# Kernel optimization log

Hardware: AMD Instinct MI355X
Metric: run time of the kernel (lower is better)

Reference implementation:

```python
import jax, jax.numpy as jnp
import numpy as np

CHAN = 24
INNER = 64
GROUPS = 8
M = 5
LAM = 1e-4
MAX_ITER = 25
BETA = 1.0
EPS = 1e-5
B, HH, WW = 128, 32, 32


def conv2d(x, w, b=None):
    # NCHW, OIHW, 3x3 SAME conv (padding = kernel//2)
    y = jax.lax.conv_general_dilated(x, w, (1, 1), 'SAME',
                                     dimension_numbers=('NCHW', 'OIHW', 'NCHW'))
    if b is not None:
        y = y + b[None, :, None, None]
    return y


def group_norm(x, g, b):
    bsz, c, h, w = x.shape
    xg = x.reshape(bsz, GROUPS, c // GROUPS, h, w)
    mu = xg.mean(axis=(2, 3, 4), keepdims=True)
    var = xg.var(axis=(2, 3, 4), keepdims=True)
    xn = ((xg - mu) / jnp.sqrt(var + EPS)).reshape(bsz, c, h, w)
    return xn * g[None, :, None, None] + b[None, :, None, None]


def batch_norm(x, g, b):
    # training-mode batch statistics over (N, H, W)
    mu = x.mean(axis=(0, 2, 3), keepdims=True)
    var = x.var(axis=(0, 2, 3), keepdims=True)
    return (x - mu) / jnp.sqrt(var + EPS) * g[None, :, None, None] + b[None, :, None, None]


def resnet_f(p, z, x):
    c1w, g1g, g1b, c2w, g2g, g2b, g3g, g3b = p
    y = group_norm(jax.nn.relu(conv2d(z, c1w)), g1g, g1b)
    return group_norm(jax.nn.relu(z + group_norm(x + conv2d(y, c2w), g2g, g2b)), g3g, g3b)


def anderson(f, x0):
    # Anderson acceleration, fixed MAX_ITER iterations (no host-sync tol break).
    bsz = x0.shape[0]
    d = x0.size // bsz
    X = jnp.zeros((bsz, M, d), x0.dtype)
    Fm = jnp.zeros((bsz, M, d), x0.dtype)
    f0 = f(x0).reshape(bsz, -1)
    X = X.at[:, 0].set(x0.reshape(bsz, -1))
    Fm = Fm.at[:, 0].set(f0)
    X = X.at[:, 1].set(f0)
    Fm = Fm.at[:, 1].set(f(f0.reshape(x0.shape)).reshape(bsz, -1))
    for k in range(2, MAX_ITER):
        n = min(k, M)
        G = Fm[:, :n] - X[:, :n]                       # [b, n, d]
        Hm = jnp.zeros((bsz, n + 1, n + 1), x0.dtype)
        Hm = Hm.at[:, 0, 1:].set(1.0).at[:, 1:, 0].set(1.0)
        Hm = Hm.at[:, 1:, 1:].set(jnp.einsum('bnd,bmd->bnm', G, G)
                                  + LAM * jnp.eye(n, dtype=x0.dtype)[None])
        yv = jnp.zeros((bsz, n + 1, 1), x0.dtype).at[:, 0, 0].set(1.0)
        alpha = jnp.linalg.solve(Hm, yv)[:, 1:, 0]     # [b, n]
        xnew = (BETA * jnp.einsum('bn,bnd->bd', alpha, Fm[:, :n])
                + (1.0 - BETA) * jnp.einsum('bn,bnd->bd', alpha, X[:, :n]))
        X = X.at[:, k % M].set(xnew)
        Fm = Fm.at[:, k % M].set(f(xnew.reshape(x0.shape)).reshape(bsz, -1))
    return X[:, (MAX_ITER - 1) % M].reshape(x0.shape)


def setup_inputs() -> dict:
    key = jax.random.key(0)
    ks = jax.random.split(key, 8)
    inp = {
        'x': jax.random.normal(ks[0], (B, 3, HH, WW), jnp.float32),
        'pre_conv_w': jax.random.normal(ks[1], (CHAN, 3, 3, 3), jnp.float32) * 0.1,
        'pre_conv_b': jnp.zeros((CHAN,), jnp.float32),
        'pre_bn_g': jnp.ones((CHAN,), jnp.float32),
        'pre_bn_b': jnp.zeros((CHAN,), jnp.float32),
        'f_conv1_w': jax.random.normal(ks[2], (INNER, CHAN, 3, 3), jnp.float32) * 0.01,
        'gn1_g': jnp.ones((INNER,), jnp.float32),
        'gn1_b': jnp.zeros((INNER,), jnp.float32),
        'f_conv2_w': jax.random.normal(ks[3], (CHAN, INNER, 3, 3), jnp.float32) * 0.01,
        'gn2_g': jnp.ones((CHAN,), jnp.float32),
        'gn2_b': jnp.zeros((CHAN,), jnp.float32),
        'gn3_g': jnp.ones((CHAN,), jnp.float32),
        'gn3_b': jnp.zeros((CHAN,), jnp.float32),
        'post_bn_g': jnp.ones((CHAN,), jnp.float32),
        'post_bn_b': jnp.zeros((CHAN,), jnp.float32),
        'fc_w': jax.random.normal(ks[4], (10, CHAN * 4 * 4), jnp.float32) * 0.05,
        'fc_b': jnp.zeros((10,), jnp.float32),
    }
    return inp


def reference(x, pre_conv_w, pre_conv_b, pre_bn_g, pre_bn_b,
              f_conv1_w, gn1_g, gn1_b, f_conv2_w, gn2_g, gn2_b, gn3_g, gn3_b,
              post_bn_g, post_bn_b, fc_w, fc_b):
    # pre: conv + BatchNorm
    xp = batch_norm(conv2d(x, pre_conv_w, pre_conv_b), pre_bn_g, pre_bn_b)
    p = (f_conv1_w, gn1_g, gn1_b, f_conv2_w, gn2_g, gn2_b, gn3_g, gn3_b)
    # DEQ fixed-point solve (eval path: train=False returns the fixed point)
    z_star = anderson(lambda z: resnet_f(p, z, xp), jnp.zeros_like(xp))
    z = resnet_f(p, z_star, xp)
    # post: relu -> BN -> avgpool(8,8) -> flatten -> linear
    h = batch_norm(jax.nn.relu(z), post_bn_g, post_bn_b)
    bsz, c, hh, ww = h.shape
    pooled = h.reshape(bsz, c, hh // 8, 8, ww // 8, 8).mean(axis=(3, 5))  # [B,C,4,4]
    return pooled.reshape(bsz, -1) @ fc_w.T + fc_b
```

## Files before the change

### kernel.cpp

```cpp
#include <hip/hip_runtime.h>
#include <hip/hip_bf16.h>

typedef __hip_bfloat16 bf16;
typedef unsigned short ushortT;
typedef __attribute__((ext_vector_type(8))) short short8;
typedef __attribute__((ext_vector_type(4))) float f32x4;

#define BB 128
#define CHAN 24
#define INNER 64
#define HW 1024
#define DD (CHAN*HW)

constexpr size_t cBD = (size_t)BB*DD;
constexpr size_t cYB = (size_t)BB*INNER*HW;

__device__ __attribute__((aligned(16))) ushortT g_xp[cBD];
__device__ __attribute__((aligned(16))) ushortT g_X[5*cBD];
__device__ __attribute__((aligned(16))) ushortT g_F[5*cBD];
__device__ __attribute__((aligned(16))) ushortT g_G[5*cBD];
__device__ __attribute__((aligned(16))) ushortT g_yb[cYB];
__device__ __attribute__((aligned(16))) ushortT g_tb[cBD];
__device__ __attribute__((aligned(16))) ushortT g_w1m[9*64*32];
__device__ __attribute__((aligned(16))) ushortT g_w2m[9*24*64];
__device__ __attribute__((aligned(16))) float g_stats2a[48];
__device__ __attribute__((aligned(16))) float g_stats2b[48];
__device__ __attribute__((aligned(16))) float g_gn1sum[BB*8*2];
__device__ __attribute__((aligned(16))) float g_gram[BB*25];
__device__ __attribute__((aligned(16))) float g_params[5120];
__device__ unsigned g_isbf16;

#define P_PCW 0
#define P_PCB 648
#define P_PBG 672
#define P_PBB 696
#define P_G1G 720
#define P_G1B 784
#define P_G2G 848
#define P_G2B 872
#define P_G3G 896
#define P_G3B 920
#define P_POG 944
#define P_POB 968
#define P_FCW 992
#define P_FCB 4832

__device__ __forceinline__ size_t aidx(int b, int icv, int pix){
  return (((size_t)b*3 + icv)*1024 + (size_t)pix)*8;
}
__device__ __forceinline__ float rdin(const void* p, int i){
  if (g_isbf16) return __bfloat162float(((const bf16*)p)[i]);
  return ((const float*)p)[i];
}
__device__ __forceinline__ float b2f(ushortT u){
  unsigned v = ((unsigned)u) << 16;
  return __builtin_bit_cast(float, v);
}
__device__ __forceinline__ ushortT f2b(float f){
  unsigned u = __builtin_bit_cast(unsigned, f);
  u += 0x7FFFu + ((u >> 16) & 1u);
  return (ushortT)(u >> 16);
}
__device__ __forceinline__ void ld24c(const ushortT* base, int b, int pix, float* o){
  #pragma unroll
  for (int icv=0;icv<3;icv++){
    short8 v = *(const short8*)&base[aidx(b,icv,pix)];
    #pragma unroll
    for (int j=0;j<8;j++) o[icv*8+j] = b2f((ushortT)v[j]);
  }
}
__device__ __forceinline__ void st24c(ushortT* base, int b, int pix, const float* i){
  #pragma unroll
  for (int icv=0;icv<3;icv++){
    short8 v;
    #pragma unroll
    for (int j=0;j<8;j++) v[j] = (short)f2b(i[icv*8+j]);
    *(short8*)&base[aidx(b,icv,pix)] = v;
  }
}

__global__ void detect_k(const void* g1g){
  if (threadIdx.x==0 && blockIdx.x==0){
    unsigned u = *(const unsigned*)g1g;
    g_isbf16 = (u == 0x3F803F80u) ? 1u : 0u;
  }
}

__global__ void cvt_params_k(const void* pcw, const void* pcb, const void* pbg, const void* pbb,
                             const void* g1g, const void* g1b, const void* g2g, const void* g2b,
                             const void* g3g, const void* g3b, const void* pog, const void* pob,
                             const void* fcw, const void* fcb){
  int t = threadIdx.x;
  for (int i=t;i<648;i+=256)  g_params[P_PCW+i]=rdin(pcw,i);
  for (int i=t;i<24;i+=256) { g_params[P_PCB+i]=rdin(pcb,i);
                              g_params[P_PBG+i]=rdin(pbg,i);
                              g_params[P_PBB+i]=rdin(pbb,i);
                              g_params[P_G2G+i]=rdin(g2g,i);
                              g_params[P_G2B+i]=rdin(g2b,i);
                              g_params[P_G3G+i]=rdin(g3g,i);
                              g_params[P_G3B+i]=rdin(g3b,i);
                              g_params[P_POG+i]=rdin(pog,i);
                              g_params[P_POB+i]=rdin(pob,i); }
  for (int i=t;i<64;i+=256) { g_params[P_G1G+i]=rdin(g1g,i);
                              g_params[P_G1B+i]=rdin(g1b,i); }
  for (int i=t;i<3840;i+=256) g_params[P_FCW+i]=rdin(fcw,i);
  for (int i=t;i<10;i+=256)   g_params[P_FCB+i]=rdin(fcb,i);
  for (int i=t;i<48;i+=256) { g_stats2a[i]=0.f; g_stats2b[i]=0.f; }
}

__global__ void wtm_k(const void* w1, const void* w2){
  int t = blockIdx.x*256 + threadIdx.x;
  if (t < 9*64*32){
    int ic = t & 31, oc = (t>>5)&63, s9 = t>>11;
    float v = (ic<24) ? rdin(w1, (oc*24+ic)*9 + s9) : 0.f;
    g_w1m[t] = f2b(v);
  }
  int u = t - 9*64*32;
  if (u >= 0 && u < 9*24*64){
    int ic = u & 63; int rest = u >> 6; int oc = rest % 24; int s9 = rest / 24;
    g_w2m[u] = f2b(rdin(w2, (oc*64+ic)*9 + s9));
  }
}

__global__ void zero0_k(){
  size_t base = ((size_t)blockIdx.x*256 + threadIdx.x)*8;
  short8 z = {0,0,0,0,0,0,0,0};
  *(short8*)&g_yb[base] = z;
  if (blockIdx.x < 1536) *(short8*)&g_X[base] = z;
  int t = blockIdx.x*256 + threadIdx.x;
  if (blockIdx.x < 8)  g_gn1sum[t] = 0.f;
}

__global__ void preconv_k(const void* __restrict__ x){
  __shared__ float sR2d[4*48];
  int id = blockIdx.x*256 + threadIdx.x;
  int b = id >> 10, pix = id & 1023;
  int yy = pix >> 5, xx = pix & 31;
  float acc[24];
  #pragma unroll
  for (int oc=0;oc<24;oc++) acc[oc] = g_params[P_PCB+oc];
  for (int ic=0; ic<3; ic++)
    for (int ky=0; ky<3; ky++){
      int gy = yy+ky-1; if (gy<0||gy>=32) continue;
      for (int kx=0;kx<3;kx++){
        int gx = xx+kx-1; if (gx<0||gx>=32) continue;
        float v = rdin(x, ((b*3+ic)*32+gy)*32+gx);
        #pragma unroll
        for (int oc=0;oc<24;oc++)
          acc[oc] += v * g_params[P_PCW+(oc*3+ic)*9+ky*3+kx];
      }
    }
  st24c(g_tb, b, pix, acc);
  int lane = threadIdx.x & 63, wv = threadIdx.x >> 6;
  #pragma unroll
  for (int c=0;c<24;c++){
    float r = acc[c], q = acc[c]*acc[c];
    #pragma unroll
    for (int off=32;off;off>>=1){ r += __shfl_down(r,off,64); q += __shfl_down(q,off,64); }
    if (lane==0){ sR2d[wv*48+c*2]=r; sR2d[wv*48+c*2+1]=q; }
  }
  __syncthreads();
  if (threadIdx.x < 48)
    atomicAdd(&g_stats2a[threadIdx.x],
      sR2d[threadIdx.x] + sR2d[48+threadIdx.x] + sR2d[96+threadIdx.x] + sR2d[144+threadIdx.x]);
}

__global__ void bn_apply_k(){
  int id = blockIdx.x*256+threadIdx.x;
  int b = id >> 10, pix = id & 1023;
  const float inv = 1.f/(BB*HW);
  float tv[24], ov[24];
  ld24c(g_tb, b, pix, tv);
  #pragma unroll
  for (int c=0;c<24;c++){
    float mean = g_stats2a[c*2]*inv;
    float var = fmaxf(g_stats2a[c*2+1]*inv - mean*mean, 0.f);
    float rstd = rsqrtf(var + 1e-5f);
    ov[c] = (tv[c]-mean)*rstd*g_params[P_PBG+c] + g_params[P_PBB+c];
  }
  st24c(g_xp, b, pix, ov);
}

__launch_bounds__(256, 2)
__global__ void conv1_k(int s){
  __shared__ ushortT sMem[29312];
  ushortT* sA = sMem;
  ushortT* sW = sMem + 10880;
  const int tid = threadIdx.x;
  const int lane = tid & 63, wv = tid >> 6;
  const int mLane = lane & 15, q = lane >> 4;
  const int b = blockIdx.x >> 2, yt = blockIdx.x & 3;
  const ushortT* __restrict__ Xs = g_X + (size_t)s*cBD;
  for (int i = tid; i < 1360; i += 256){
    int icv = i & 3, apix = i >> 2;
    int yl = apix / 34, xl = apix - yl*34;
    int gy = yt*8 - 1 + yl, gx = xl - 1;
    short8 v = {0,0,0,0,0,0,0,0};
    if (gy >= 0 && gy < 32 && gx >= 0 && gx < 32 && icv < 3)
      v = *(const short8*)&Xs[aidx(b, icv, gy*32 + gx)];
    *(short8*)&sA[(size_t)(apix*4 + (icv ^ (apix&3)))*8] = v;
  }
  for (int i = tid; i < 2304; i += 256){
    int icv = i & 3, rest = i >> 2;
    int oc = rest & 63, s9 = rest >> 6;
    short8 v = *(const short8*)&g_w1m[(size_t)((s9*64 + oc)*32) + icv*8];
    *(short8*)&sW[(size_t)((s9*64+oc)*4 + (icv ^ (oc&3)))*8] = v;
  }
  __syncthreads();
  f32x4 acc[4][4];
  #pragma unroll
  for (int mt=0;mt<4;mt++)
    #pragma unroll
    for (int nt=0;nt<4;nt++) acc[mt][nt] = (f32x4){0.f,0.f,0.f,0.f};
  for (int s9=0; s9<9; s9++){
    int ky = s9/3, kx = s9 - ky*3;
    short8 bfr[4];
    #pragma unroll
    for (int nt=0;nt<4;nt++){
      int oc = nt*16 + mLane;
      bfr[nt] = *(const short8*)&sW[(size_t)((s9*64+oc)*4 + (q ^ (oc&3)))*8];
    }
    #pragma unroll
    for (int mt=0;mt<4;mt++){
      int g = wv*4+mt;
      int apix = ((g>>1) + ky)*34 + (g&1)*16 + mLane + kx;
      short8 afr = *(const short8*)&sA[(size_t)(apix*4 + (q ^ (apix&3)))*8];
      #pragma unroll
      for (int nt=0;nt<4;nt++)
        acc[mt][nt] = __builtin_amdgcn_mfma_f32_16x16x32_bf16(afr, bfr[nt], acc[mt][nt], 0,0,0);
    }
  }
  __syncthreads();
  ushortT* sOut = sMem;
  #pragma unroll
  for (int mt=0;mt<4;mt++){
    int g = wv*4+mt;
    #pragma unroll
    for (int nt=0;nt<4;nt++){
      int oc = nt*16 + mLane;
      #pragma unroll
      for (int r=0;r<4;r++){
        int pix = (g>>1)*32 + (g&1)*16 + q*4 + r;
        sOut[pix*64 + oc] = f2b(fmaxf(acc[mt][nt][r], 0.f));
      }
    }
  }
  __syncthreads();
  float s0=0.f, s1=0.f;
  size_t gbase = ((size_t)b*1024 + yt*256)*64;
  for (int c = tid; c < 2048; c += 256){
    short8 v = *(const short8*)&sOut[c*8];
    *(short8*)&g_yb[gbase + (size_t)c*8] = v;
    #pragma unroll
    for (int j=0;j<8;j++){ float f = b2f((ushortT)v[j]); s0 += f; s1 += f*f; }
  }
  s0 += __shfl_down(s0,32); s1 += __shfl_down(s1,32);
  s0 += __shfl_down(s0,16); s1 += __shfl_down(s1,16);
  s0 += __shfl_down(s0, 8); s1 += __shfl_down(s1, 8);
  if (lane < 8){
    atomicAdd(&g_gn1sum[(b*8+lane)*2],   s0);
    atomicAdd(&g_gn1sum[(b*8+lane)*2+1], s1);
  }
}

template<int N>
__device__ __forceinline__ void chol_alpha(const float Kf[5][5], float* alpha){
  double K[N][N];
  #pragma unroll
  for (int i=0;i<N;i++)
    #pragma unroll
    for (int j=0;j<N;j++)
      K[i][j] = (double)Kf[i][j] + (i==j ? 1e-4 : 0.0);
  #pragma unroll
  for (int c=0;c<N;c++){
    double d = K[c][c];
    #pragma unroll
    for (int k2=0;k2<c;k2++) d -= K[c][k2]*K[c][k2];
    d = sqrt(fmax(d, 1e-300));
    K[c][c] = d;
    double inv = 1.0/d;
    #pragma unroll
    for (int r=c+1;r<N;r++){
      double v = K[r][c];
      #pragma unroll
      for (int k2=0;k2<c;k2++) v -= K[r][k2]*K[c][k2];
      K[r][c] = v*inv;
    }
  }
  double y[N];
  #pragma unroll
  for (int i=0;i<N;i++){
    double v = 1.0;
    #pragma unroll
    for (int j=0;j<i;j++) v -= K[i][j]*y[j];
    y[i] = v / K[i][i];
  }
  double w[N];
  #pragma unroll
  for (int i=N-1;i>=0;i--){
    double v = y[i];
    #pragma unroll
    for (int j=i+1;j<N;j++) v -= K[j][i]*w[j];
    w[i] = v / K[i][i];
  }
  double sum = 0.0;
  #pragma unroll
  for (int i=0;i<N;i++) sum += w[i];
  double invs = 1.0/sum;
  #pragma unroll
  for (int i=0;i<N;i++) alpha[i] = (float)(w[i]*invs);
}

#define C2F_SMEM 161440

__launch_bounds__(1024)
__global__ void c2f_k(int s, int n, int snext){
  extern __shared__ __align__(16) ushortT sU[];
  ushortT* sYb = sU;
  ushortT* sTB = sU;
  ushortT* sW2 = sU + 65536;
  float* sS    = (float*)(sU + 79360);
  float* sAff1  = sS;
  float* sStat2 = sS + 128;
  float* sAff2  = sS + 176;
  float* sStat3 = sS + 224;
  float* sAff3  = sS + 240;
  float* sRed   = sS + 288;
  float* sRedG  = sS + 544;
  float* sAlpha = sS + 624;
  float* sFin   = (float*)sTB;

  const int b = blockIdx.x;
  const int t = threadIdx.x;
  const int lane = t & 63, wv = t >> 6;
  const int mLane = lane & 15, q = lane >> 4;
  const int g0 = wv*4;
  const bool ntOK = (mLane < 8);
  const bool fin = (n == 0);

  if (t < 64){
    const int c = t, gr = c>>3;
    float S = g_gn1sum[(b*8+gr)*2], Q = g_gn1sum[(b*8+gr)*2+1];
    float mean = S*(1.f/8192.f);
    float var  = fmaxf(Q*(1.f/8192.f) - mean*mean, 0.f);
    float rstd = rsqrtf(var + 1e-5f);
    float sc = rstd*g_params[P_G1G+c];
    sAff1[c] = sc; sAff1[64+c] = g_params[P_G1B+c] - mean*sc;
  }
  if (t < 16) g_gn1sum[b*16 + t] = 0.f;
  if (t >= 64 && t < 112) sStat2[t-64] = 0.f;
  if (t >= 112 && t < 128) sStat3[t-112] = 0.f;
  __syncthreads();

  for (int i=t; i<8192; i+=1024){
    int chk = i & 7, pix = i >> 3;
    short8 raw = *(const short8*)&g_yb[((size_t)b*1024 + pix)*64 + chk*8];
    short8 v;
    #pragma unroll
    for (int j=0;j<8;j++){
      int c = chk*8+j;
      v[j] = (short)f2b(b2f((ushortT)raw[j])*sAff1[c] + sAff1[64+c]);
    }
    *(short8*)&sYb[(size_t)(pix*8 + (chk^(pix&7)))*8] = v;
  }
  for (int i=t; i<1728; i+=1024){
    int icv=i&7, rest=i>>3, oc=rest%24, s9=rest/24;
    *(short8*)&sW2[(size_t)((s9*24+oc)*8 + (icv^(oc&7)))*8] =
      *(const short8*)&g_w2m[(size_t)((s9*24+oc)*64) + icv*8];
  }
  __syncthreads();

  f32x4 a2[4][2];
  #pragma unroll
  for (int mt=0;mt<4;mt++){ a2[mt][0]=(f32x4){0.f,0.f,0.f,0.f}; a2[mt][1]=(f32x4){0.f,0.f,0.f,0.f}; }
  for (int s9=0; s9<9; ++s9){
    const int ky = s9/3, kx = s9 - ky*3;
    #pragma unroll
    for (int ks=0; ks<2; ++ks){
      const int ch = ks*4 + q;
      short8 b0 = *(const short8*)&sW2[(size_t)((s9*24+mLane)*8 + (ch^(mLane&7)))*8];
      short8 b1 = ntOK ? *(const short8*)&sW2[(size_t)((s9*24+16+mLane)*8 + (ch^(mLane&7)))*8]
                       : (short8){0,0,0,0,0,0,0,0};
      #pragma unroll
      for (int mt=0;mt<4;mt++){
        const int g = g0+mt;
        const int gy = (g>>1) + ky - 1;
        const int gx = (g&1)*16 + mLane + kx - 1;
        short8 afr = {0,0,0,0,0,0,0,0};
        if (gy>=0 && gy<32 && gx>=0 && gx<32){
          const int pp = gy*32 + gx;
          afr = *(const short8*)&sYb[(size_t)(pp*8 + (ch^(pp&7)))*8];
        }
        a2[mt][0] = __builtin_amdgcn_mfma_f32_16x16x32_bf16(afr, b0, a2[mt][0], 0,0,0);
        a2[mt][1] = __builtin_amdgcn_mfma_f32_16x16x32_bf16(afr, b1, a2[mt][1], 0,0,0);
      }
    }
  }
  #pragma unroll
  for (int ci=0; ci<2; ++ci){
    const int oc = ci*16 + mLane;
    const bool ok = (ci==0) || ntOK;
    const int icv = oc>>3, e = oc&7;
    float s0=0.f, s1=0.f;
    if (ok){
      #pragma unroll
      for (int mt=0;mt<4;mt++){
        #pragma unroll
        for (int r=0;r<4;r++){
          const int pp = (g0+mt)*16 + q*4 + r;
          float v = a2[mt][ci][r] + b2f(g_xp[aidx(b,icv,pp)+e]);
          a2[mt][ci][r] = v;
          s0 += v; s1 += v*v;
        }
      }
    }
    s0 += __shfl_down(s0,32); s1 += __shfl_down(s1,32);
    s0 += __shfl_down(s0,16); s1 += __shfl_down(s1,16);
    if (lane < 16 && ok){
      atomicAdd(&sStat2[oc*2],   s0);
      atomicAdd(&sStat2[oc*2+1], s1);
    }
  }
  __syncthreads();

  #pragma unroll
  for (int ci=0; ci<2; ++ci){
    const int oc = ci*16 + mLane;
    if ((ci==0) || ntOK){
      const int icv = oc>>3, e = oc&7;
      #pragma unroll
      for (int mt=0;mt<4;mt++)
        #pragma unroll
        for (int r=0;r<4;r++){
          const int pp = (g0+mt)*16 + q*4 + r;
          sTB[(size_t)(pp*4 + (icv ^ ((pp>>2)&3)))*8 + e] = f2b(a2[mt][ci][r]);
        }
    }
  }
  if (t < 24){
    const int gr = t/3;
    float S = sStat2[(gr*3)*2]  +sStat2[(gr*3+1)*2]  +sStat2[(gr*3+2)*2];
    float Q = sStat2[(gr*3)*2+1]+sStat2[(gr*3+1)*2+1]+sStat2[(gr*3+2)*2+1];
    float m = S*(1.f/3072.f);
    float rstd = rsqrtf(fmaxf(Q*(1.f/3072.f)-m*m,0.f)+1e-5f);
    float sc = rstd*g_params[P_G2G+t];
    sAff2[t] = sc; sAff2[24+t] = g_params[P_G2B+t] - m*sc;
  }
  __syncthreads();

  float v[24], xv[24];
  #pragma unroll
  for (int i=0;i<3;i++){
    short8 t8 = *(const short8*)&sTB[(size_t)(t*4 + (i ^ ((t>>2)&3)))*8];
    #pragma unroll
    for (int j8=0;j8<8;j8++) v[i*8+j8] = b2f((ushortT)t8[j8]);
  }
  ld24c(g_X + (size_t)s*cBD, b, t, xv);
  float p0[8], p1[8];
  #pragma unroll
  for (int g=0;g<8;g++){ p0[g]=0.f; p1[g]=0.f; }
  #pragma unroll
  for (int c=0;c<24;c++){
    float val = fmaxf(xv[c] + v[c]*sAff2[c] + sAff2[24+c], 0.f);
    v[c] = val;
    int g = c/3;
    p0[g] += val; p1[g] += val*val;
  }
  #pragma unroll
  for (int g=0;g<8;g++){
    #pragma unroll
    for (int off=32;off;off>>=1){ p0[g]+=__shfl_down(p0[g],off,64); p1[g]+=__shfl_down(p1[g],off,64); }
  }
  if (lane==0){
    #pragma unroll
    for (int g=0;g<8;g++){ sRed[wv*16+g*2]=p0[g]; sRed[wv*16+g*2+1]=p1[g]; }
  }
  __syncthreads();
  if (t < 8){
    float S=0.f, Q=0.f;
    #pragma unroll
    for (int w=0;w<16;w++){ S += sRed[w*16+t*2]; Q += sRed[w*16+t*2+1]; }
    float m = S*(1.f/3072.f);
    sStat3[t*2]   = m;
    sStat3[t*2+1] = rsqrtf(fmaxf(Q*(1.f/3072.f) - m*m, 0.f) + 1e-5f);
  }
  __syncthreads();
  if (t < 24){
    int g = t/3;
    float sc = sStat3[g*2+1]*g_params[P_G3G+t];
    sAff3[t] = sc; sAff3[24+t] = g_params[P_G3B+t] - sStat3[g*2]*sc;
  }
  __syncthreads();
  float fv[24];
  #pragma unroll
  for (int c=0;c<24;c++) fv[c] = v[c]*sAff3[c] + sAff3[24+c];
  st24c(g_F + (size_t)s*cBD, b, t, fv);

  if (!fin){
    float gl[24];
    #pragma unroll
    for (int c=0;c<24;c++) gl[c] = b2f(f2b(fv[c] - xv[c]));
    st24c(g_G + (size_t)s*cBD, b, t, gl);
    float part[5];
    #pragma unroll
    for (int j=0;j<5;j++) part[j]=0.f;
    #pragma unroll
    for (int j=0;j<5;j++){
      if (j < n){
        float acc=0.f;
        if (j == s){
          #pragma unroll
          for (int c=0;c<24;c++) acc += gl[c]*gl[c];
        } else {
          float gv[24];
          ld24c(g_G + (size_t)j*cBD, b, t, gv);
          #pragma unroll
          for (int c=0;c<24;c++) acc += gl[c]*gv[c];
        }
        part[j] = acc;
      }
    }
    #pragma unroll
    for (int j=0;j<5;j++){
      float vv = part[j];
      #pragma unroll
      for (int off=32;off;off>>=1) vv += __shfl_down(vv,off,64);
      if (lane==0) sRedG[wv*5+j] = vv;
    }
    __syncthreads();
    if (t == 0){
      for (int j=0;j<n;j++){
        float vv = 0.f;
        for (int w=0;w<16;w++) vv += sRedG[w*5+j];
        g_gram[b*25+s*5+j] = vv;
        g_gram[b*25+j*5+s] = vv;
      }
      float Kf[5][5];
      for (int i=0;i<n;i++)
        for (int j=0;j<n;j++) Kf[i][j] = g_gram[b*25+i*5+j];
      float al[5];
      if (n==1) al[0]=1.f;
      else if (n==2) chol_alpha<2>(Kf, al);
      else if (n==3) chol_alpha<3>(Kf, al);
      else if (n==4) chol_alpha<4>(Kf, al);
      else chol_alpha<5>(Kf, al);
      for (int j=0;j<n;j++) sAlpha[j] = al[j];
    }
    __syncthreads();
    float al[5];
    #pragma unroll
    for (int j=0;j<5;j++) al[j] = (j<n) ? sAlpha[j] : 0.f;
    float xn[24];
    #pragma unroll
    for (int c=0;c<24;c++) xn[c] = 0.f;
    #pragma unroll
    for (int j=0;j<5;j++){
      if (j < n){
        if (j == s){
          #pragma unroll
          for (int c=0;c<24;c++) xn[c] += al[j]*b2f(f2b(fv[c]));
        } else {
          float fv2[24];
          ld24c(g_F + (size_t)j*cBD, b, t, fv2);
          #pragma unroll
          for (int c=0;c<24;c++) xn[c] += al[j]*fv2[c];
        }
      }
    }
    st24c(g_X + (size_t)snext*cBD, b, t, xn);
  } else {
    #pragma unroll
    for (int c=0;c<24;c++){
      float r = fmaxf(b2f(f2b(fv[c])), 0.f);
      float q2 = r*r;
      #pragma unroll
      for (int off=32;off;off>>=1){ r += __shfl_down(r,off,64); q2 += __shfl_down(q2,off,64); }
      if (lane==0){ sFin[wv*48+c*2]=r; sFin[wv*48+c*2+1]=q2; }
    }
    __syncthreads();
    if (t < 48){
      float vv = 0.f;
      #pragma unroll
      for (int w=0;w<16;w++) vv += sFin[w*48+t];
      atomicAdd(&g_stats2b[t], vv);
    }
  }
}

__global__ void postfc_k(void* __restrict__ out){
  __shared__ float sPool[384];
  __shared__ float sMean[24], sRstd[24];
  int b = blockIdx.x, t = threadIdx.x;
  if (t < 24){
    const float inv = 1.f/(BB*HW);
    float mean = g_stats2b[t*2]*inv;
    float var = fmaxf(g_stats2b[t*2+1]*inv - mean*mean, 0.f);
    sMean[t] = mean; sRstd[t] = rsqrtf(var + 1e-5f);
  }
  __syncthreads();
  const ushortT* z = g_F + 4*cBD;
  for (int i=t; i<384; i+=256){
    int c = i>>4, bin = i&15, ph = bin>>2, pw = bin&3;
    int icv = c>>3, e = c&7;
    float gg = g_params[P_POG+c], bv = g_params[P_POB+c];
    float mean = sMean[c], rstd = sRstd[c];
    float sum = 0.f;
    for (int dy=0;dy<8;dy++)
      for (int dx=0;dx<8;dx++){
        int pix = (ph*8+dy)*32 + pw*8+dx;
        float vv = fmaxf(b2f(z[aidx(b,icv,pix) + e]), 0.f);
        sum += (vv-mean)*rstd*gg + bv;
      }
    sPool[i] = sum*(1.f/64.f);
  }
  __syncthreads();
  if (t < 10){
    float s2 = g_params[P_FCB+t];
    for (int k2=0;k2<384;k2++) s2 += sPool[k2]*g_params[P_FCW+t*384+k2];
    if (g_isbf16) ((bf16*)out)[b*10+t] = __float2bfloat16(s2);
    else ((float*)out)[b*10+t] = s2;
  }
}

extern "C" void kernel_launch(void* const* d_in, const int* in_sizes, int n_in,
                              void* d_out, int out_size, void* d_ws, size_t ws_size,
                              hipStream_t stream){
  const void* x   = d_in[0];
  const void* pcw = d_in[1];
  const void* pcb = d_in[2];
  const void* pbg = d_in[3];
  const void* pbb = d_in[4];
  const void* w1  = d_in[5];
  const void* g1g = d_in[6];
  const void* g1b = d_in[7];
  const void* w2  = d_in[8];
  const void* g2g = d_in[9];
  const void* g2b = d_in[10];
  const void* g3g = d_in[11];
  const void* g3b = d_in[12];
  const void* pog = d_in[13];
  const void* pob = d_in[14];
  const void* fcw = d_in[15];
  const void* fcb = d_in[16];
  (void)d_ws; (void)ws_size; (void)in_sizes; (void)n_in; (void)out_size;

  static bool attrSet = false;
  if (!attrSet){
    hipFuncSetAttribute(reinterpret_cast<const void*>(c2f_k),
                        hipFuncAttributeMaxDynamicSharedMemorySize, C2F_SMEM);
    attrSet = true;
  }

  detect_k<<<1,64,0,stream>>>(g1g);
  cvt_params_k<<<1,256,0,stream>>>(pcw,pcb,pbg,pbb,g1g,g1b,g2g,g2b,g3g,g3b,pog,pob,fcw,fcb);
  wtm_k<<<126,256,0,stream>>>(w1, w2);

  preconv_k<<<512,256,0,stream>>>(x);
  bn_apply_k<<<512,256,0,stream>>>();

  zero0_k<<<4096,256,0,stream>>>();
  c2f_k<<<128,1024,C2F_SMEM,stream>>>(0, 1, 1);

  for (int k=1;k<25;k++){
    int s = k%5;
    conv1_k<<<512,256,0,stream>>>(s);
    if (k < 24){
      int n = (k+1 < 5) ? (k+1) : 5;
      c2f_k<<<128,1024,C2F_SMEM,stream>>>(s, n, (k+1)%5);
    } else {
      c2f_k<<<128,1024,C2F_SMEM,stream>>>(s, 0, 0);
    }
  }

  postfc_k<<<128,256,0,stream>>>(d_out);
}
```

Baseline: 1.382 ms.

## Fuse Anderson mixing into conv1 prologue and retile xp for coalesced residual loads

The Anderson mixing step, which forms the new iterate as an alpha-weighted sum of the stored F history, moves out of the tail of c2f_k and into conv1_k's input-tile load. c2f_k now writes only the alphas to global memory, and conv1_k recomputes the combination per halo tile, writing the non-halo part to a single g_xcur buffer in place of the 5-slot X history. Separately, g_xp is stored in a pixel-group tiled layout so c2f_k can read the residual with 4-wide vector loads instead of scattered scalar loads. The cost is extra redundant F reads for halo pixels in conv1, which are loaded and mixed by neighbouring blocks as well.

```diff
diff --git a/kernel.cpp b/kernel.cpp
--- a/kernel.cpp
+++ b/kernel.cpp
@@ -4,6 +4,7 @@
 typedef __hip_bfloat16 bf16;
 typedef unsigned short ushortT;
 typedef __attribute__((ext_vector_type(8))) short short8;
+typedef __attribute__((ext_vector_type(4))) short s16x4;
 typedef __attribute__((ext_vector_type(4))) float f32x4;
 
 #define BB 128
@@ -16,7 +17,7 @@
 constexpr size_t cYB = (size_t)BB*INNER*HW;
 
 __device__ __attribute__((aligned(16))) ushortT g_xp[cBD];
-__device__ __attribute__((aligned(16))) ushortT g_X[5*cBD];
+__device__ __attribute__((aligned(16))) ushortT g_xcur[cBD];
 __device__ __attribute__((aligned(16))) ushortT g_F[5*cBD];
 __device__ __attribute__((aligned(16))) ushortT g_G[5*cBD];
 __device__ __attribute__((aligned(16))) ushortT g_yb[cYB];
@@ -27,6 +28,7 @@
 __device__ __attribute__((aligned(16))) float g_stats2b[48];
 __device__ __attribute__((aligned(16))) float g_gn1sum[BB*8*2];
 __device__ __attribute__((aligned(16))) float g_gram[BB*25];
+__device__ __attribute__((aligned(16))) float g_alpha[BB*8];
 __device__ __attribute__((aligned(16))) float g_params[5120];
 __device__ unsigned g_isbf16;
 
@@ -47,6 +49,9 @@
 
 __device__ __forceinline__ size_t aidx(int b, int icv, int pix){
   return (((size_t)b*3 + icv)*1024 + (size_t)pix)*8;
+}
+__device__ __forceinline__ size_t tidx(int b, int g, int c, int p){
+  return ((((size_t)b*64 + g)*24 + c)<<4) + p;
 }
 __device__ __forceinline__ float rdin(const void* p, int i){
   if (g_isbf16) return __bfloat162float(((const bf16*)p)[i]);
@@ -126,7 +131,7 @@
   size_t base = ((size_t)blockIdx.x*256 + threadIdx.x)*8;
   short8 z = {0,0,0,0,0,0,0,0};
   *(short8*)&g_yb[base] = z;
-  if (blockIdx.x < 1536) *(short8*)&g_X[base] = z;
+  if (blockIdx.x < 1536) *(short8*)&g_xcur[base] = z;
   int t = blockIdx.x*256 + threadIdx.x;
   if (blockIdx.x < 8)  g_gn1sum[t] = 0.f;
 }
@@ -169,20 +174,21 @@
   int id = blockIdx.x*256+threadIdx.x;
   int b = id >> 10, pix = id & 1023;
   const float inv = 1.f/(BB*HW);
-  float tv[24], ov[24];
+  float tv[24];
   ld24c(g_tb, b, pix, tv);
+  int g = pix >> 4, p = pix & 15;
   #pragma unroll
   for (int c=0;c<24;c++){
     float mean = g_stats2a[c*2]*inv;
     float var = fmaxf(g_stats2a[c*2+1]*inv - mean*mean, 0.f);
     float rstd = rsqrtf(var + 1e-5f);
-    ov[c] = (tv[c]-mean)*rstd*g_params[P_PBG+c] + g_params[P_PBB+c];
-  }
-  st24c(g_xp, b, pix, ov);
+    float ov = (tv[c]-mean)*rstd*g_params[P_PBG+c] + g_params[P_PBB+c];
+    g_xp[tidx(b,g,c,p)] = f2b(ov);
+  }
 }
 
 __launch_bounds__(256, 2)
-__global__ void conv1_k(int s){
+__global__ void conv1_k(int na){
   __shared__ ushortT sMem[29312];
   ushortT* sA = sMem;
   ushortT* sW = sMem + 10880;
@@ -190,14 +196,30 @@
   const int lane = tid & 63, wv = tid >> 6;
   const int mLane = lane & 15, q = lane >> 4;
   const int b = blockIdx.x >> 2, yt = blockIdx.x & 3;
-  const ushortT* __restrict__ Xs = g_X + (size_t)s*cBD;
+  float al[5];
+  #pragma unroll
+  for (int j=0;j<5;j++) al[j] = (j<na) ? g_alpha[b*8+j] : 0.f;
   for (int i = tid; i < 1360; i += 256){
     int icv = i & 3, apix = i >> 2;
     int yl = apix / 34, xl = apix - yl*34;
     int gy = yt*8 - 1 + yl, gx = xl - 1;
     short8 v = {0,0,0,0,0,0,0,0};
-    if (gy >= 0 && gy < 32 && gx >= 0 && gx < 32 && icv < 3)
-      v = *(const short8*)&Xs[aidx(b, icv, gy*32 + gx)];
+    if (gy >= 0 && gy < 32 && gx >= 0 && gx < 32 && icv < 3){
+      int pix = gy*32 + gx;
+      float acc[8] = {0.f,0.f,0.f,0.f,0.f,0.f,0.f,0.f};
+      #pragma unroll
+      for (int j=0;j<5;j++){
+        if (j < na){
+          short8 f = *(const short8*)&g_F[(size_t)j*cBD + aidx(b,icv,pix)];
+          #pragma unroll
+          for (int e=0;e<8;e++) acc[e] += al[j]*b2f((ushortT)f[e]);
+        }
+      }
+      #pragma unroll
+      for (int e=0;e<8;e++) v[e] = (short)f2b(acc[e]);
+      if (yl >= 1 && yl < 9 && xl >= 1 && xl < 33)
+        *(short8*)&g_xcur[aidx(b,icv,pix)] = v;
+    }
     *(short8*)&sA[(size_t)(apix*4 + (icv ^ (apix&3)))*8] = v;
   }
   for (int i = tid; i < 2304; i += 256){
@@ -314,7 +336,7 @@
 #define C2F_SMEM 161440
 
 __launch_bounds__(1024)
-__global__ void c2f_k(int s, int n, int snext){
+__global__ void c2f_k(int s, int n){
   extern __shared__ __align__(16) ushortT sU[];
   ushortT* sYb = sU;
   ushortT* sTB = sU;
@@ -327,7 +349,6 @@
   float* sAff3  = sS + 240;
   float* sRed   = sS + 288;
   float* sRedG  = sS + 544;
-  float* sAlpha = sS + 624;
   float* sFin   = (float*)sTB;
 
   const int b = blockIdx.x;
@@ -400,15 +421,14 @@
   for (int ci=0; ci<2; ++ci){
     const int oc = ci*16 + mLane;
     const bool ok = (ci==0) || ntOK;
-    const int icv = oc>>3, e = oc&7;
     float s0=0.f, s1=0.f;
     if (ok){
       #pragma unroll
       for (int mt=0;mt<4;mt++){
+        s16x4 xpv = *(const s16x4*)&g_xp[tidx(b, g0+mt, oc, q*4)];
         #pragma unroll
         for (int r=0;r<4;r++){
-          const int pp = (g0+mt)*16 + q*4 + r;
-          float v = a2[mt][ci][r] + b2f(g_xp[aidx(b,icv,pp)+e]);
+          float v = a2[mt][ci][r] + b2f((ushortT)xpv[r]);
           a2[mt][ci][r] = v;
           s0 += v; s1 += v*v;
         }
@@ -455,7 +475,7 @@
     #pragma unroll
     for (int j8=0;j8<8;j8++) v[i*8+j8] = b2f((ushortT)t8[j8]);
   }
-  ld24c(g_X + (size_t)s*cBD, b, t, xv);
+  ld24c(g_xcur, b, t, xv);
   float p0[8], p1[8];
   #pragma unroll
   for (int g=0;g<8;g++){ p0[g]=0.f; p1[g]=0.f; }
@@ -544,30 +564,8 @@
       else if (n==3) chol_alpha<3>(Kf, al);
       else if (n==4) chol_alpha<4>(Kf, al);
       else chol_alpha<5>(Kf, al);
-      for (int j=0;j<n;j++) sAlpha[j] = al[j];
-    }
-    __syncthreads();
-    float al[5];
-    #pragma unroll
-    for (int j=0;j<5;j++) al[j] = (j<n) ? sAlpha[j] : 0.f;
-    float xn[24];
-    #pragma unroll
-    for (int c=0;c<24;c++) xn[c] = 0.f;
-    #pragma unroll
-    for (int j=0;j<5;j++){
-      if (j < n){
-        if (j == s){
-          #pragma unroll
-          for (int c=0;c<24;c++) xn[c] += al[j]*b2f(f2b(fv[c]));
-        } else {
-          float fv2[24];
-          ld24c(g_F + (size_t)j*cBD, b, t, fv2);
-          #pragma unroll
-          for (int c=0;c<24;c++) xn[c] += al[j]*fv2[c];
-        }
-      }
-    }
-    st24c(g_X + (size_t)snext*cBD, b, t, xn);
+      for (int j=0;j<n;j++) g_alpha[b*8+j] = al[j];
+    }
   } else {
     #pragma unroll
     for (int c=0;c<24;c++){
@@ -659,16 +657,17 @@
   bn_apply_k<<<512,256,0,stream>>>();
 
   zero0_k<<<4096,256,0,stream>>>();
-  c2f_k<<<128,1024,C2F_SMEM,stream>>>(0, 1, 1);
+  c2f_k<<<128,1024,C2F_SMEM,stream>>>(0, 1);
 
   for (int k=1;k<25;k++){
     int s = k%5;
-    conv1_k<<<512,256,0,stream>>>(s);
+    int na = (k < 5) ? k : 5;
+    conv1_k<<<512,256,0,stream>>>(na);
     if (k < 24){
       int n = (k+1 < 5) ? (k+1) : 5;
-      c2f_k<<<128,1024,C2F_SMEM,stream>>>(s, n, (k+1)%5);
+      c2f_k<<<128,1024,C2F_SMEM,stream>>>(s, n);
     } else {
-      c2f_k<<<128,1024,C2F_SMEM,stream>>>(s, 0, 0);
+      c2f_k<<<128,1024,C2F_SMEM,stream>>>(s, 0);
     }
   }
 
```

Result: slower. 1.466 ms (+6.0%).
